# Kernel optimization log

Hardware: AMD Instinct MI355X
Metric: run time of the kernel (lower is better)

The kernel has to match this reference:

```python
import jax, jax.numpy as jnp
import numpy as np

DIM = 256
HEADS = 8
HD = DIM // HEADS  # 32
RPE_H = 512
STRIDE = 16
B, NQ = 4, 300
HH, WW = 64, 64
N = HH * WW


def setup_inputs() -> dict:
    key = jax.random.key(0)
    ks = jax.random.split(key, 24)

    def lin(k, fan_in, fan_out):
        return (jax.random.normal(k, (fan_in, fan_out), jnp.float32)
                / np.float32(np.sqrt(fan_in)))

    # boxes in absolute pixel coords (image is WW*STRIDE = 1024 px wide)
    rp_xy = jax.random.uniform(ks[0], (B, NQ, 1, 2), jnp.float32) * (WW * STRIDE)
    rp_wh = jax.random.uniform(ks[1], (B, NQ, 1, 2), jnp.float32) * 256.0 + 16.0
    reference_points = jnp.concatenate([rp_xy, rp_wh], axis=-1)  # [B,NQ,1,4]

    inp = {
        "query": jax.random.normal(ks[2], (B, NQ, DIM), jnp.float32),
        "reference_points": reference_points,
        "k_input_flatten": jax.random.normal(ks[3], (B, N, DIM), jnp.float32),
        "v_input_flatten": jax.random.normal(ks[4], (B, N, DIM), jnp.float32),
        "input_spatial_shapes": jnp.array([[HH, WW]], dtype=jnp.int32),
        "input_padding_mask": (jax.random.uniform(ks[5], (B, N)) < 0.1).astype(jnp.int32),
        # projections (stored as [in, out]; y = x @ W + b)
        "Wq": lin(ks[6], DIM, DIM), "bq": jnp.zeros((DIM,), jnp.float32),
        "Wk": lin(ks[7], DIM, DIM), "bk": jnp.zeros((DIM,), jnp.float32),
        "Wv": lin(ks[8], DIM, DIM), "bv": jnp.zeros((DIM,), jnp.float32),
        "Wp": lin(ks[9], DIM, DIM), "bp": jnp.zeros((DIM,), jnp.float32),
        # CPB MLP 1 (x-deltas): Linear(2,512)+ReLU+Linear(512,HEADS,no bias)
        "W1x": lin(ks[10], 2, RPE_H), "b1x": jnp.zeros((RPE_H,), jnp.float32),
        "W2x": lin(ks[11], RPE_H, HEADS),
        # CPB MLP 2 (y-deltas)
        "W1y": lin(ks[12], 2, RPE_H), "b1y": jnp.zeros((RPE_H,), jnp.float32),
        "W2y": lin(ks[13], RPE_H, HEADS),
    }
    return inp


def reference(query, reference_points, k_input_flatten, v_input_flatten,
              input_spatial_shapes, input_padding_mask,
              Wq, bq, Wk, bk, Wv, bv, Wp, bp,
              W1x, b1x, W2x, W1y, b1y, W2y):
    h = int(input_spatial_shapes[0, 0])
    w = int(input_spatial_shapes[0, 1])
    scale = HD ** -0.5

    # cxcywh -> (x1,y1,x2,y2)
    c, s = reference_points[..., :2], reference_points[..., 2:]
    ref_pts = jnp.concatenate([c - s / 2, c + s / 2], axis=-1)  # [B,NQ,1,4]

    pos_x = (jnp.arange(w, dtype=jnp.float32) + 0.5) * STRIDE  # [w]
    pos_y = (jnp.arange(h, dtype=jnp.float32) + 0.5) * STRIDE  # [h]
    delta_x = ref_pts[..., 0::2] - pos_x[None, None, :, None]  # [B,NQ,w,2]
    delta_y = ref_pts[..., 1::2] - pos_y[None, None, :, None]  # [B,NQ,h,2]

    rpe_x = jax.nn.relu(delta_x @ W1x + b1x) @ W2x  # [B,NQ,w,HEADS]
    rpe_y = jax.nn.relu(delta_y @ W1y + b1y) @ W2y  # [B,NQ,h,HEADS]
    rpe = rpe_x[:, :, None, :, :] + rpe_y[:, :, :, None, :]  # [B,NQ,h,w,H]

    Bq, Nq, C = query.shape
    rpe = rpe.reshape(Bq, Nq, h * w, HEADS).transpose(0, 3, 1, 2)  # [B,H,NQ,N]

    q = (query @ Wq + bq).reshape(Bq, Nq, HEADS, HD).transpose(0, 2, 1, 3) * scale
    k = (k_input_flatten @ Wk + bk).reshape(Bq, -1, HEADS, HD).transpose(0, 2, 1, 3)
    v = (v_input_flatten @ Wv + bv).reshape(Bq, -1, HEADS, HD).transpose(0, 2, 1, 3)

    attn = jnp.einsum('bhqd,bhkd->bhqk', q, k) + rpe
    attn = attn + input_padding_mask[:, None, None, :].astype(attn.dtype) * (-100.0)
    fi = jnp.finfo(attn.dtype)
    attn = jnp.clip(attn, fi.min, fi.max)
    attn = jax.nn.softmax(attn, axis=-1)

    x = jnp.einsum('bhqk,bhkd->bhqd', attn, v)
    x = x.transpose(0, 2, 1, 3).reshape(Bq, Nq, C)
    return x @ Wp + bp
```

## Files before the change

### kernel.cpp

```cpp
#include <hip/hip_runtime.h>
#include <math.h>

#define B_   4
#define NQ_  300
#define DIM_ 256
#define H_   8
#define HD_  32
#define N_   4096

typedef _Float16 f16;
typedef f16   f16x8 __attribute__((ext_vector_type(8)));
typedef f16   f16x4 __attribute__((ext_vector_type(4)));
typedef float f32x4 __attribute__((ext_vector_type(4)));

__global__ __launch_bounds__(256) void prep_wt(
    const float* __restrict__ Wq, const float* __restrict__ Wk,
    const float* __restrict__ Wv, const float* __restrict__ Wp,
    f16* __restrict__ WT, float qscale)
{
  __shared__ float t[64][65];
  const int z = blockIdx.z;
  const float* W = z == 0 ? Wq : z == 1 ? Wk : z == 2 ? Wv : Wp;
  const float s = z == 0 ? qscale : 1.0f;
  f16* O = WT + (size_t)z * 65536;
  const int k0 = blockIdx.y * 64, n0 = blockIdx.x * 64;
  const int r = threadIdx.x >> 2, c0 = (threadIdx.x & 3) * 16;
#pragma unroll
  for (int c = 0; c < 16; c += 4) {
    float4 v = *(const float4*)(W + (size_t)(k0 + r) * 256 + n0 + c0 + c);
    t[r][c0 + c] = v.x; t[r][c0 + c + 1] = v.y;
    t[r][c0 + c + 2] = v.z; t[r][c0 + c + 3] = v.w;
  }
  __syncthreads();
  f16* orow = O + (size_t)(n0 + r) * 256 + k0 + c0;
#pragma unroll
  for (int c = 0; c < 16; c += 4) {
    f16x4 p;
    p[0] = (f16)(t[c0 + c + 0][r] * s);
    p[1] = (f16)(t[c0 + c + 1][r] * s);
    p[2] = (f16)(t[c0 + c + 2][r] * s);
    p[3] = (f16)(t[c0 + c + 3][r] * s);
    *(f16x4*)(orow + c) = p;
  }
}

__device__ __forceinline__ void gemm_body(
    const void* __restrict__ Ain, const f16* __restrict__ WT,
    const float* __restrict__ bias, void* __restrict__ C,
    int M, float scale, int a_f16, int mode, int bm, int bn, int nbt, int tid)
{
  __shared__ f16 As[64][40];
  __shared__ f16 Bs[4][64][40];
  const int lane = tid & 63;
  const int wv = tid >> 6;
  const int l15 = lane & 15, g = lane >> 4;
  const int arow = tid >> 2, akq = (tid & 3) * 8;

  f32x4 acc[4][4];
#pragma unroll
  for (int t = 0; t < 4; ++t)
#pragma unroll
    for (int nt = 0; nt < 4; ++nt) acc[t][nt] = (f32x4){0.f, 0.f, 0.f, 0.f};

  for (int k0 = 0; k0 < 256; k0 += 32) {
    {
      const int gm = bm + arow;
      f16x8 av;
      if (gm < M) {
        if (a_f16 == 2) {
          const int bb2 = gm / NQ_, qq2 = gm % NQ_;
          const int kk = k0 + akq;
          av = *(const f16x8*)((const f16*)Ain +
              (((size_t)(bb2 * H_ + (kk >> 5)) * NQ_) + qq2) * 32 + (kk & 31));
        } else if (a_f16 == 1) {
          av = *(const f16x8*)((const f16*)Ain + (size_t)gm * 256 + k0 + akq);
        } else {
          const float* ap = (const float*)Ain + (size_t)gm * 256 + k0 + akq;
          float4 a0 = *(const float4*)ap;
          float4 a1 = *(const float4*)(ap + 4);
          av[0] = (f16)a0.x; av[1] = (f16)a0.y; av[2] = (f16)a0.z; av[3] = (f16)a0.w;
          av[4] = (f16)a1.x; av[5] = (f16)a1.y; av[6] = (f16)a1.z; av[7] = (f16)a1.w;
        }
      } else {
#pragma unroll
        for (int i = 0; i < 8; ++i) av[i] = (f16)0.f;
      }
      *(f16x8*)&As[arow][akq] = av;
      for (int t = 0; t < nbt; ++t)
        *(f16x8*)&Bs[t][arow][akq] =
            *(const f16x8*)(WT + (size_t)(bn + t * 64 + arow) * 256 + k0 + akq);
    }
    __syncthreads();
    const f16x8 af = *(const f16x8*)&As[wv * 16 + l15][g * 8];
    for (int t = 0; t < nbt; ++t) {
#pragma unroll
      for (int nt = 0; nt < 4; ++nt) {
        const f16x8 bf = *(const f16x8*)&Bs[t][nt * 16 + l15][g * 8];
        acc[t][nt] = __builtin_amdgcn_mfma_f32_16x16x32_f16(af, bf, acc[t][nt], 0, 0, 0);
      }
    }
    __syncthreads();
  }

  for (int t = 0; t < nbt; ++t) {
#pragma unroll
    for (int nt = 0; nt < 4; ++nt) {
      const int n = bn + t * 64 + nt * 16 + l15;
      const float bv = bias[n] * scale;
      if (mode == 2) {
        const int m0 = bm + wv * 16 + g * 4;
        const int bb = m0 >> 12, nk = m0 & 4095;
        f16x4 pk;
#pragma unroll
        for (int r = 0; r < 4; ++r) pk[r] = (f16)(acc[t][nt][r] + bv);
        *(f16x4*)((f16*)C + (size_t)bb * (256 * 4096) + (size_t)n * 4096 + nk) = pk;
      } else {
#pragma unroll
        for (int r = 0; r < 4; ++r) {
          const int m = bm + wv * 16 + g * 4 + r;
          if (m >= M) continue;
          const float v = acc[t][nt][r] + bv;
          if (mode == 0)      ((float*)C)[(size_t)m * 256 + n] = v;
          else if (mode == 1) ((f16*)C)[(size_t)m * 256 + n] = (f16)v;
          else                ((f16*)C)[((((size_t)(m >> 12)) * H_ + (n >> 5)) * N_
                                         + (m & 4095)) * 32 + (n & 31)] = (f16)v;
        }
      }
    }
  }
}

__global__ __launch_bounds__(256) void proj_qkv(
    const float* __restrict__ query, const float* __restrict__ kin,
    const float* __restrict__ vin, const f16* __restrict__ WT,
    const float* __restrict__ bq, const float* __restrict__ bk,
    const float* __restrict__ bv, f16* __restrict__ Qf,
    f16* __restrict__ Kf, f16* __restrict__ Vtf, float qscale)
{
  const int bid = blockIdx.x;
  const int lg  = (bid & 7) * 96 + (bid >> 3);
  const int z   = lg >> 8;
  const int bm  = (lg & 255) * 64;
  if (z == 0) {
    if (bm >= B_ * NQ_) return;
    gemm_body(query, WT, bq, Qf, B_ * NQ_, qscale, 0, 1, bm, 0, 4, threadIdx.x);
  } else if (z == 1) {
    gemm_body(kin, WT + 65536, bk, Kf, B_ * N_, 1.0f, 0, 3, bm, 0, 4, threadIdx.x);
  } else {
    gemm_body(vin, WT + 2 * 65536, bv, Vtf, B_ * N_, 1.0f, 0, 2, bm, 0, 4, threadIdx.x);
  }
}

__global__ __launch_bounds__(256) void gemm_out(
    const f16* __restrict__ X, const f16* __restrict__ WT,
    const float* __restrict__ bp, float* __restrict__ out)
{
  gemm_body(X, WT + 3 * 65536, bp, out, B_ * NQ_, 1.0f, 2, 0,
            blockIdx.y * 64, blockIdx.x * 64, 1, threadIdx.x);
}

__global__ __launch_bounds__(256) void rpe_kernel(
    const float* __restrict__ refpts,
    const float* __restrict__ W1x, const float* __restrict__ b1x, const float* __restrict__ W2x,
    const float* __restrict__ W1y, const float* __restrict__ b1y, const float* __restrict__ W2y,
    float* __restrict__ rpx, float* __restrict__ rpy)
{
  __shared__ float sRed[4][64][9];
  const int tid = threadIdx.x;
  const int lane = tid & 63;
  const int wv = __builtin_amdgcn_readfirstlane(tid >> 6);
  const int bq = blockIdx.x;
  const int axis = blockIdx.y;
  const float* W1 = axis ? W1y : W1x;
  const float* b1 = axis ? b1y : b1x;
  const float* W2 = axis ? W2y : W2x;
  float* out = axis ? rpy : rpx;

  const float c  = refpts[bq * 4 + axis];
  const float sz = refpts[bq * 4 + 2 + axis];
  const float pos = (lane + 0.5f) * 16.0f;
  const float d0 = c - 0.5f * sz - pos;
  const float d1 = c + 0.5f * sz - pos;
  float acc[8] = {};
  const int r0 = wv * 128;
#pragma unroll 4
  for (int i = 0; i < 128; ++i) {
    const int r = r0 + i;
    const float w10 = W1[r], w11 = W1[512 + r], bb = b1[r];
    const float hv = fmaxf(fmaf(d0, w10, fmaf(d1, w11, bb)), 0.0f);
    const float* w2r = W2 + r * 8;
#pragma unroll
    for (int hh = 0; hh < 8; ++hh) acc[hh] += hv * w2r[hh];
  }
#pragma unroll
  for (int hh = 0; hh < 8; ++hh) sRed[wv][lane][hh] = acc[hh];
  __syncthreads();
  for (int idx = tid; idx < 512; idx += 256) {
    const int hh = idx >> 6, jj = idx & 63;
    out[(size_t)bq * 512 + idx] =
        sRed[0][jj][hh] + sRed[1][jj][hh] + sRed[2][jj][hh] + sRed[3][jj][hh];
  }
}

__global__ __launch_bounds__(512, 4) void attn_mfma(
    const f16* __restrict__ Qf, const f16* __restrict__ Kf,
    const f16* __restrict__ Vtf, const float* __restrict__ rpx,
    const float* __restrict__ rpy, const int* __restrict__ mask,
    f16* __restrict__ X)
{
  __shared__ float smask[N_];
  __shared__ float srx[16][68];
  __shared__ float sry[16][68];
  __shared__ float mO[7][8][64];
  __shared__ float mlm[7][16];
  __shared__ float mll[7][16];

  const int tid = threadIdx.x;
  const int lane = tid & 63;
  const int kh = tid >> 6;
  const int bid = blockIdx.x;
  const int lg  = (bid & 7) * 80 + (bid >> 3);
  const int qg = lg % 20;
  const int h  = (lg / 20) % H_;
  const int b  = lg / (20 * H_);
  const int q0 = qg * 16;
  const float L2E = 1.44269504f;

  {
    const int4* mm4 = (const int4*)(mask + b * N_);
    for (int i = tid; i < N_ / 4; i += 512) {
      int4 mm = mm4[i];
      smask[4 * i + 0] = -100.f * L2E * (float)mm.x;
      smask[4 * i + 1] = -100.f * L2E * (float)mm.y;
      smask[4 * i + 2] = -100.f * L2E * (float)mm.z;
      smask[4 * i + 3] = -100.f * L2E * (float)mm.w;
    }
  }
  for (int i = tid; i < 1024; i += 512) {
    int qq = i >> 6, j = i & 63;
    int qg2 = q0 + qq; if (qg2 > NQ_ - 1) qg2 = NQ_ - 1;
    size_t base = (size_t)(b * NQ_ + qg2) * 512 + (size_t)h * 64 + j;
    srx[qq][j] = rpx[base] * L2E;
    sry[qq][j] = rpy[base] * L2E;
  }
  __syncthreads();

  const int l15 = lane & 15, g = lane >> 4;
  const int qrow0 = q0 + l15;
  const int qa = qrow0 > NQ_ - 1 ? NQ_ - 1 : qrow0;

  const f16x8 qf0 = *(const f16x8*)(Qf + (size_t)(b * NQ_ + qa) * 256 + h * 32 + g * 8);

  f32x4 O00 = {0.f,0.f,0.f,0.f}, O01 = {0.f,0.f,0.f,0.f};
  float lacc0 = 0.f;
  float mrun0 = -1e30f;
  const f16* kb  = Kf + (size_t)(b * H_ + h) * N_ * 32 + g * 8;
  const f16* v0p = Vtf + (size_t)(b * 256 + h * 32 + l15) * N_ + g * 4;
  const f16* v1p = v0p + (size_t)16 * N_;

  for (int sp = 0; sp < 8; ++sp) {
    const int kbase = kh * 512 + sp * 64;
    f16x8 kf[4];
    f16x4 va[4], vb[4];
#pragma unroll
    for (int cc = 0; cc < 4; ++cc) {
      kf[cc] = *(const f16x8*)(kb + (size_t)(kbase + cc * 16 + l15) * 32);
      va[cc] = *(const f16x4*)(v0p + kbase + cc * 16);
      vb[cc] = *(const f16x4*)(v1p + kbase + cc * 16);
    }
    f32x4 s0[4];
    float lm0 = -1e30f;
#pragma unroll
    for (int cc = 0; cc < 4; ++cc) {
      const int k0 = kbase + cc * 16;
      f32x4 S0 = __builtin_amdgcn_mfma_f32_16x16x32_f16(
          kf[cc], qf0, (f32x4){0.f,0.f,0.f,0.f}, 0, 0, 0);
      const float ry0 = sry[l15][k0 >> 6];
      const float4 rx0 = *(const float4*)&srx[l15][(k0 & 63) + g * 4];
      const float4 sm = *(const float4*)&smask[k0 + g * 4];
      s0[cc][0] = fmaf(S0[0], L2E, rx0.x + sm.x + ry0);
      s0[cc][1] = fmaf(S0[1], L2E, rx0.y + sm.y + ry0);
      s0[cc][2] = fmaf(S0[2], L2E, rx0.z + sm.z + ry0);
      s0[cc][3] = fmaf(S0[3], L2E, rx0.w + sm.w + ry0);
      lm0 = fmaxf(lm0, fmaxf(fmaxf(s0[cc][0], s0[cc][1]), fmaxf(s0[cc][2], s0[cc][3])));
    }
    lm0 = fmaxf(lm0, __shfl_xor(lm0, 16));
    lm0 = fmaxf(lm0, __shfl_xor(lm0, 32));
    const float mn0 = fmaxf(mrun0, lm0);
    const float f0 = exp2f(mrun0 - mn0);
    mrun0 = mn0;
    lacc0 *= f0;
#pragma unroll
    for (int r = 0; r < 4; ++r) { O00[r] *= f0; O01[r] *= f0; }
#pragma unroll
    for (int cc = 0; cc < 4; ++cc) {
      f16x4 pf0;
#pragma unroll
      for (int r = 0; r < 4; ++r) {
        const float p0 = exp2f(s0[cc][r] - mrun0);
        lacc0 += p0;
        pf0[r] = (f16)p0;
      }
      O00 = __builtin_amdgcn_mfma_f32_16x16x16f16(va[cc], pf0, O00, 0, 0, 0);
      O01 = __builtin_amdgcn_mfma_f32_16x16x16f16(vb[cc], pf0, O01, 0, 0, 0);
    }
  }

  lacc0 += __shfl_xor(lacc0, 16); lacc0 += __shfl_xor(lacc0, 32);

  if (kh > 0) {
#pragma unroll
    for (int r = 0; r < 4; ++r) {
      mO[kh - 1][r][lane]     = O00[r];
      mO[kh - 1][4 + r][lane] = O01[r];
    }
    if (lane < 16) {
      mlm[kh - 1][lane] = mrun0;
      mll[kh - 1][lane] = lacc0;
    }
  }
  __syncthreads();
  if (kh == 0) {
    float ms = mrun0;
#pragma unroll
    for (int w = 0; w < 7; ++w) ms = fmaxf(ms, mlm[w][l15]);
    const float fme = exp2f(mrun0 - ms);
    float lt = lacc0 * fme;
    float fw[7];
#pragma unroll
    for (int w = 0; w < 7; ++w) {
      fw[w] = exp2f(mlm[w][l15] - ms);
      lt += mll[w][l15] * fw[w];
    }
    const float rl = 1.0f / lt;
    if (qrow0 < NQ_) {
      f16* xr = X + ((size_t)(b * H_ + h) * NQ_ + qrow0) * 32;
      f16x4 p0, p1;
#pragma unroll
      for (int r = 0; r < 4; ++r) {
        float o0 = O00[r] * fme, o1 = O01[r] * fme;
#pragma unroll
        for (int w = 0; w < 7; ++w) {
          o0 += mO[w][r][lane] * fw[w];
          o1 += mO[w][4 + r][lane] * fw[w];
        }
        p0[r] = (f16)(o0 * rl);
        p1[r] = (f16)(o1 * rl);
      }
      *(f16x4*)(xr + g * 4) = p0;
      *(f16x4*)(xr + 16 + g * 4) = p1;
    }
  }
}

extern "C" void kernel_launch(void* const* d_in, const int* in_sizes, int n_in,
                              void* d_out, int out_size, void* d_ws, size_t ws_size,
                              hipStream_t stream)
{
  const float* query  = (const float*)d_in[0];
  const float* refpts = (const float*)d_in[1];
  const float* kin    = (const float*)d_in[2];
  const float* vin    = (const float*)d_in[3];
  const int*   mask   = (const int*)d_in[5];
  const float* Wq = (const float*)d_in[6];
  const float* bq = (const float*)d_in[7];
  const float* Wk = (const float*)d_in[8];
  const float* bk = (const float*)d_in[9];
  const float* Wv = (const float*)d_in[10];
  const float* bv = (const float*)d_in[11];
  const float* Wp = (const float*)d_in[12];
  const float* bp = (const float*)d_in[13];
  const float* W1x = (const float*)d_in[14];
  const float* b1x = (const float*)d_in[15];
  const float* W2x = (const float*)d_in[16];
  const float* W1y = (const float*)d_in[17];
  const float* b1y = (const float*)d_in[18];
  const float* W2y = (const float*)d_in[19];

  char* wsb = (char*)d_ws;
  f16*   Qf  = (f16*)(wsb);
  f16*   Kf  = (f16*)(wsb + 622592);
  f16*   Vtf = (f16*)(wsb + 9011200);
  float* rpx = (float*)(wsb + 17399808);
  float* rpy = (float*)(wsb + 19857408);
  f16*   X   = (f16*)(wsb + 22315008);
  f16*   WT  = (f16*)(wsb + 22937600);

  const float scale = 0.17677669529663687f;

  hipLaunchKernelGGL(prep_wt, dim3(4, 4, 4), dim3(256), 0, stream,
                     Wq, Wk, Wv, Wp, WT, scale);
  hipLaunchKernelGGL(rpe_kernel, dim3(B_ * NQ_, 2), dim3(256), 0, stream,
                     refpts, W1x, b1x, W2x, W1y, b1y, W2y, rpx, rpy);
  hipLaunchKernelGGL(proj_qkv, dim3(768), dim3(256), 0, stream,
                     query, kin, vin, WT, bq, bk, bv, Qf, Kf, Vtf, scale);
  hipLaunchKernelGGL(attn_mfma, dim3(B_ * H_ * 20), dim3(512), 0, stream,
                     Qf, Kf, Vtf, rpx, rpy, mask, X);
  hipLaunchKernelGGL(gemm_out, dim3(4, 19), dim3(256), 0, stream,
                     X, WT, bp, (float*)d_out);
}
```

Baseline: 228.8 us.

## Store V head-major like K and transpose V tiles through shared memory

The V projection now writes the same [B,H,N,32] head-major layout as K instead of a transposed [B,256,N] layout. The transposed V store was a strided scatter. In the attention kernel, each wave loads a contiguous 64x32 V chunk with 16-byte loads, writes it to a padded per-wave LDS tile, and reads back per-lane f16x4 operands for the PV MFMA. The tile shares a union with the merge buffers to limit LDS growth. This trades strided 8-byte global V loads and the transposed projection store for extra LDS traffic and scalar LDS reads. There is no barrier between a wave's LDS writes and reads beyond wave-level ordering, and the per-wave tile is reused across iterations.

```diff
diff --git a/kernel.cpp b/kernel.cpp
--- a/kernel.cpp
+++ b/kernel.cpp
@@ -107,24 +107,15 @@
     for (int nt = 0; nt < 4; ++nt) {
       const int n = bn + t * 64 + nt * 16 + l15;
       const float bv = bias[n] * scale;
-      if (mode == 2) {
-        const int m0 = bm + wv * 16 + g * 4;
-        const int bb = m0 >> 12, nk = m0 & 4095;
-        f16x4 pk;
-#pragma unroll
-        for (int r = 0; r < 4; ++r) pk[r] = (f16)(acc[t][nt][r] + bv);
-        *(f16x4*)((f16*)C + (size_t)bb * (256 * 4096) + (size_t)n * 4096 + nk) = pk;
-      } else {
-#pragma unroll
-        for (int r = 0; r < 4; ++r) {
-          const int m = bm + wv * 16 + g * 4 + r;
-          if (m >= M) continue;
-          const float v = acc[t][nt][r] + bv;
-          if (mode == 0)      ((float*)C)[(size_t)m * 256 + n] = v;
-          else if (mode == 1) ((f16*)C)[(size_t)m * 256 + n] = (f16)v;
-          else                ((f16*)C)[((((size_t)(m >> 12)) * H_ + (n >> 5)) * N_
-                                         + (m & 4095)) * 32 + (n & 31)] = (f16)v;
-        }
+#pragma unroll
+      for (int r = 0; r < 4; ++r) {
+        const int m = bm + wv * 16 + g * 4 + r;
+        if (m >= M) continue;
+        const float v = acc[t][nt][r] + bv;
+        if (mode == 0)      ((float*)C)[(size_t)m * 256 + n] = v;
+        else if (mode == 1) ((f16*)C)[(size_t)m * 256 + n] = (f16)v;
+        else                ((f16*)C)[((((size_t)(m >> 12)) * H_ + (n >> 5)) * N_
+                                       + (m & 4095)) * 32 + (n & 31)] = (f16)v;
       }
     }
   }
@@ -147,7 +138,7 @@
   } else if (z == 1) {
     gemm_body(kin, WT + 65536, bk, Kf, B_ * N_, 1.0f, 0, 3, bm, 0, 4, threadIdx.x);
   } else {
-    gemm_body(vin, WT + 2 * 65536, bv, Vtf, B_ * N_, 1.0f, 0, 2, bm, 0, 4, threadIdx.x);
+    gemm_body(vin, WT + 2 * 65536, bv, Vtf, B_ * N_, 1.0f, 0, 3, bm, 0, 4, threadIdx.x);
   }
 }
 
@@ -211,9 +202,14 @@
   __shared__ float smask[N_];
   __shared__ float srx[16][68];
   __shared__ float sry[16][68];
-  __shared__ float mO[7][8][64];
-  __shared__ float mlm[7][16];
-  __shared__ float mll[7][16];
+  __shared__ union {
+    f16 vtile[8][64 * 36];
+    struct {
+      float mO[7][8][64];
+      float mlm[7][16];
+      float mll[7][16];
+    } m;
+  } ovl;
 
   const int tid = threadIdx.x;
   const int lane = tid & 63;
@@ -254,20 +250,21 @@
   f32x4 O00 = {0.f,0.f,0.f,0.f}, O01 = {0.f,0.f,0.f,0.f};
   float lacc0 = 0.f;
   float mrun0 = -1e30f;
-  const f16* kb  = Kf + (size_t)(b * H_ + h) * N_ * 32 + g * 8;
-  const f16* v0p = Vtf + (size_t)(b * 256 + h * 32 + l15) * N_ + g * 4;
-  const f16* v1p = v0p + (size_t)16 * N_;
+  const f16* kb = Kf  + (size_t)(b * H_ + h) * N_ * 32 + g * 8;
+  const f16* vb = Vtf + (size_t)(b * H_ + h) * N_ * 32;
+  f16* vt = &ovl.vtile[kh][0];
 
   for (int sp = 0; sp < 8; ++sp) {
     const int kbase = kh * 512 + sp * 64;
     f16x8 kf[4];
-    f16x4 va[4], vb[4];
-#pragma unroll
-    for (int cc = 0; cc < 4; ++cc) {
+#pragma unroll
+    for (int cc = 0; cc < 4; ++cc)
       kf[cc] = *(const f16x8*)(kb + (size_t)(kbase + cc * 16 + l15) * 32);
-      va[cc] = *(const f16x4*)(v0p + kbase + cc * 16);
-      vb[cc] = *(const f16x4*)(v1p + kbase + cc * 16);
-    }
+    const f16* vsrc = vb + (size_t)kbase * 32;
+    f16x8 vv[4];
+#pragma unroll
+    for (int c = 0; c < 4; ++c)
+      vv[c] = *(const f16x8*)(vsrc + c * 512 + lane * 8);
     f32x4 s0[4];
     float lm0 = -1e30f;
 #pragma unroll
@@ -284,6 +281,15 @@
       s0[cc][3] = fmaf(S0[3], L2E, rx0.w + sm.w + ry0);
       lm0 = fmaxf(lm0, fmaxf(fmaxf(s0[cc][0], s0[cc][1]), fmaxf(s0[cc][2], s0[cc][3])));
     }
+#pragma unroll
+    for (int c = 0; c < 4; ++c) {
+      const int row = c * 16 + (lane >> 2), d0 = (lane & 3) * 8;
+      f16x4 lo, hi;
+#pragma unroll
+      for (int i = 0; i < 4; ++i) { lo[i] = vv[c][i]; hi[i] = vv[c][4 + i]; }
+      *(f16x4*)&vt[row * 36 + d0]     = lo;
+      *(f16x4*)&vt[row * 36 + d0 + 4] = hi;
+    }
     lm0 = fmaxf(lm0, __shfl_xor(lm0, 16));
     lm0 = fmaxf(lm0, __shfl_xor(lm0, 32));
     const float mn0 = fmaxf(mrun0, lm0);
@@ -301,36 +307,44 @@
         lacc0 += p0;
         pf0[r] = (f16)p0;
       }
-      O00 = __builtin_amdgcn_mfma_f32_16x16x16f16(va[cc], pf0, O00, 0, 0, 0);
-      O01 = __builtin_amdgcn_mfma_f32_16x16x16f16(vb[cc], pf0, O01, 0, 0, 0);
+      f16x4 va_, vb_;
+#pragma unroll
+      for (int i = 0; i < 4; ++i) {
+        const int krow = cc * 16 + g * 4 + i;
+        va_[i] = vt[krow * 36 + l15];
+        vb_[i] = vt[krow * 36 + 16 + l15];
+      }
+      O00 = __builtin_amdgcn_mfma_f32_16x16x16f16(va_, pf0, O00, 0, 0, 0);
+      O01 = __builtin_amdgcn_mfma_f32_16x16x16f16(vb_, pf0, O01, 0, 0, 0);
     }
   }
 
   lacc0 += __shfl_xor(lacc0, 16); lacc0 += __shfl_xor(lacc0, 32);
 
+  __syncthreads();
   if (kh > 0) {
 #pragma unroll
     for (int r = 0; r < 4; ++r) {
-      mO[kh - 1][r][lane]     = O00[r];
-      mO[kh - 1][4 + r][lane] = O01[r];
+      ovl.m.mO[kh - 1][r][lane]     = O00[r];
+      ovl.m.mO[kh - 1][4 + r][lane] = O01[r];
     }
     if (lane < 16) {
-      mlm[kh - 1][lane] = mrun0;
-      mll[kh - 1][lane] = lacc0;
+      ovl.m.mlm[kh - 1][lane] = mrun0;
+      ovl.m.mll[kh - 1][lane] = lacc0;
     }
   }
   __syncthreads();
   if (kh == 0) {
     float ms = mrun0;
 #pragma unroll
-    for (int w = 0; w < 7; ++w) ms = fmaxf(ms, mlm[w][l15]);
+    for (int w = 0; w < 7; ++w) ms = fmaxf(ms, ovl.m.mlm[w][l15]);
     const float fme = exp2f(mrun0 - ms);
     float lt = lacc0 * fme;
     float fw[7];
 #pragma unroll
     for (int w = 0; w < 7; ++w) {
-      fw[w] = exp2f(mlm[w][l15] - ms);
-      lt += mll[w][l15] * fw[w];
+      fw[w] = exp2f(ovl.m.mlm[w][l15] - ms);
+      lt += ovl.m.mll[w][l15] * fw[w];
     }
     const float rl = 1.0f / lt;
     if (qrow0 < NQ_) {
@@ -341,8 +355,8 @@
         float o0 = O00[r] * fme, o1 = O01[r] * fme;
 #pragma unroll
         for (int w = 0; w < 7; ++w) {
-          o0 += mO[w][r][lane] * fw[w];
-          o1 += mO[w][4 + r][lane] * fw[w];
+          o0 += ovl.m.mO[w][r][lane] * fw[w];
+          o1 += ovl.m.mO[w][4 + r][lane] * fw[w];
         }
         p0[r] = (f16)(o0 * rl);
         p1[r] = (f16)(o1 * rl);
```

Result: faster. 202.5 us, median of 2 (-11.5%).
